# Kernel optimization log

Hardware: AMD Instinct MI355X
Metric: run time of the kernel (lower is better)

The kernel has to match this reference:

```python
import jax, jax.numpy as jnp
import numpy as np

B, S, D, H, G = 2, 4096, 768, 12, 64
HD = D // H
W = 256              # one-sided window (attention_window=512); also the chunk size
NC = S // W
NEG = -1e9
SCALE = 1.0 / np.sqrt(HD)


def setup_inputs() -> dict:
    key = jax.random.key(0)
    ks = jax.random.split(key, 9)
    lin = lambda k: 0.02 * jax.random.normal(k, (D, D), dtype=jnp.float32)
    zb = lambda: jnp.zeros((D,), jnp.float32)
    return {
        "query": jax.random.normal(ks[0], (S, B, D), dtype=jnp.float32),
        # 0 = local token, -1 = global token (wrapper multiplies by -1 -> +1 = global in HF convention)
        "key_padding_mask": jnp.zeros((B, S), jnp.int32).at[:, :G].set(-1),
        "Wq": lin(ks[1]), "bq": zb(),
        "Wk": lin(ks[2]), "bk": zb(),
        "Wv": lin(ks[3]), "bv": zb(),
        "Wqg": lin(ks[4]), "bqg": zb(),
        "Wkg": lin(ks[5]), "bkg": zb(),
        "Wvg": lin(ks[6]), "bvg": zb(),
        "Wo": lin(ks[7]), "bo": zb(),
    }


def _heads(x):  # [B,S,D] -> [B,H,S,HD]
    return x.reshape(B, S, H, HD).transpose(0, 2, 1, 3)


def reference(query, key_padding_mask, Wq, bq, Wk, bk, Wv, bv,
              Wqg, bqg, Wkg, bkg, Wvg, bvg, Wo, bo):
    x = query.transpose(1, 0, 2)                      # [B,S,D]
    attn_mask = -key_padding_mask                     # wrapper: key_padding_mask * -1
    is_pad = attn_mask < 0                            # [B,S]
    is_glb = attn_mask > 0

    q = _heads(x @ Wq + bq) * SCALE                   # [B,H,S,HD]
    k = _heads(x @ Wk + bk)
    v = _heads(x @ Wv + bv)

    # ---- sliding-window scores via overlapping 3-chunk key blocks ----
    qc = q.reshape(B, H, NC, W, HD)
    blk_idx = jnp.arange(NC)[:, None] * W + jnp.arange(3 * W)[None, :]   # [NC,3W] into padded seq
    kpad = jnp.pad(k, ((0, 0), (0, 0), (W, W), (0, 0)))
    vpad = jnp.pad(v, ((0, 0), (0, 0), (W, W), (0, 0)))
    kblk = kpad[:, :, blk_idx]                        # [B,H,NC,3W,HD]
    vblk = vpad[:, :, blk_idx]
    local = jnp.einsum('bhcqd,bhckd->bhcqk', qc, kblk)  # [B,H,NC,W,3W]

    rel = jnp.arange(3 * W)[None, :] - jnp.arange(W)[:, None] - W        # key pos - query pos
    jpos = (jnp.arange(NC)[:, None, None] - 1) * W + jnp.arange(3 * W)[None, None, :]
    band_ok = (jnp.abs(rel)[None] <= W) & (jpos >= 0) & (jpos < S)       # [NC,W,3W]

    key_bad = is_pad | is_glb                         # pad keys masked; global keys handled separately
    kb_blk = jnp.pad(key_bad, ((0, 0), (W, W)), constant_values=True)[:, blk_idx]  # [B,NC,3W]
    ok = band_ok[None, None] & ~kb_blk[:, None, :, None, :]
    local = jnp.where(ok, local, NEG)

    # ---- all queries -> global keys (first G tokens), regular K/V ----
    gsc = jnp.einsum('bhqd,bhgd->bhqg', q, k[:, :, :G])                  # [B,H,S,G]

    scores = jnp.concatenate([gsc, local.reshape(B, H, S, 3 * W)], axis=-1)
    probs = jax.nn.softmax(scores, axis=-1)
    pg = probs[..., :G]
    pl = probs[..., G:].reshape(B, H, NC, W, 3 * W)

    out = jnp.einsum('bhcqk,bhckd->bhcqd', pl, vblk).reshape(B, H, S, HD)
    out = out + jnp.einsum('bhqg,bhgd->bhqd', pg, v[:, :, :G])

    # ---- global query rows: full attention with the dedicated global projections ----
    qg = (_heads(x @ Wqg + bqg) * SCALE)[:, :, :G]    # [B,H,G,HD]
    kg = _heads(x @ Wkg + bkg)
    vg = _heads(x @ Wvg + bvg)
    gq = jnp.einsum('bhgd,bhkd->bhgk', qg, kg)        # [B,H,G,S]
    gq = jnp.where(is_pad[:, None, None, :], NEG, gq)
    gp = jax.nn.softmax(gq, axis=-1)
    out = out.at[:, :, :G].set(jnp.einsum('bhgk,bhkd->bhgd', gp, vg))

    attn_out = out.transpose(0, 2, 1, 3).reshape(B, S, D)   # merge heads -> [B,S,D]
    attn_out = attn_out.transpose(1, 0, 2)                  # back to [S,B,D]
    return attn_out @ Wo + bo                               # wrapper's output Linear
```

## Files before the change

kernel.cpp:

```cpp
#include <hip/hip_runtime.h>
#include <hip/hip_bf16.h>
#include <cstdint>

#define BB 2
#define SS 4096
#define DD 768
#define HH 12
#define GG 64
#define WW 256

typedef __hip_bfloat16 bf16;
typedef unsigned short u16;
typedef __attribute__((ext_vector_type(8))) short short8v;
typedef __attribute__((ext_vector_type(4))) float floatx4;
typedef __attribute__((ext_vector_type(16))) float floatx16;

#define QSCALE 0.18033688011112042f

__device__ __forceinline__ float b2f(u16 u) {
  return __uint_as_float(((unsigned int)u) << 16);
}
__device__ __forceinline__ u16 f2bu(float f) {
  bf16 h = __float2bfloat16(f);
  return *reinterpret_cast<u16*>(&h);
}
__device__ __forceinline__ void async_copy16(const u16* g, u16* l) {
  __builtin_amdgcn_global_load_lds(
      (const __attribute__((address_space(1))) void*)g,
      (__attribute__((address_space(3))) void*)l, 16, 0, 0);
}

struct P7 { const void* p[7]; };

__global__ __launch_bounds__(256) void detect_dtype(const u16* __restrict__ q,
                                                    int* __restrict__ flag) {
  __shared__ int cnt;
  int tid = threadIdx.x;
  if (tid == 0) cnt = 0;
  __syncthreads();
  int bad = 0;
#pragma unroll
  for (int i = 0; i < 16; ++i) {
    float f = b2f(q[tid * 16 + i]);
    if (!isfinite(f) || fabsf(f) > 100.f) bad++;
  }
  atomicAdd(&cnt, bad);
  __syncthreads();
  if (tid == 0) *flag = (cnt > 256) ? 1 : 0;
}

__global__ __launch_bounds__(256) void prep(P7 wsrc, P7 bsrc,
                                            const void* __restrict__ qsrc,
                                            bf16* __restrict__ cWt,
                                            bf16* __restrict__ cB,
                                            bf16* __restrict__ cQ,
                                            const int* __restrict__ flag) {
  bool f32 = (*flag != 0);
  int z = blockIdx.z;
  if (z < 7) {
    __shared__ float tile[32][33];
    const void* src = wsrc.p[z];
    bf16* d = cWt + (size_t)z * DD * DD;
    int tx = threadIdx.x & 31, ty = threadIdx.x >> 5;
    int k0 = blockIdx.x * 32, n0 = blockIdx.y * 32;
#pragma unroll
    for (int i = 0; i < 32; i += 8) {
      int k = k0 + ty + i, n = n0 + tx;
      float v = f32 ? ((const float*)src)[(size_t)k * DD + n]
                    : b2f(((const u16*)src)[(size_t)k * DD + n]);
      tile[ty + i][tx] = v;
    }
    __syncthreads();
#pragma unroll
    for (int i = 0; i < 32; i += 8) {
      int n = n0 + ty + i, k = k0 + tx;
      d[(size_t)n * DD + k] = __float2bfloat16(tile[tx][ty + i]);
    }
  } else if (z == 7) {
    int bidx = blockIdx.x + 24 * blockIdx.y;
    const int n = BB * HH * SS * 64;
    for (int i = bidx * 256 + threadIdx.x; i < n; i += 576 * 256) {
      float v = f32 ? ((const float*)qsrc)[i] : b2f(((const u16*)qsrc)[i]);
      cQ[i] = __float2bfloat16(v);
    }
  } else {
    int which = blockIdx.x;
    if (which >= 7 || blockIdx.y != 0) return;
    const void* s = bsrc.p[which];
    for (int j = threadIdx.x; j < DD; j += 256)
      cB[which * DD + j] =
          __float2bfloat16(f32 ? ((const float*)s)[j] : b2f(((const u16*)s)[j]));
  }
}

__global__ __launch_bounds__(256) void tr_vt2(const bf16* __restrict__ s0,
                                              bf16* __restrict__ d0,
                                              const bf16* __restrict__ s1,
                                              bf16* __restrict__ d1) {
  __shared__ u16 T[64][66];
  int stile = blockIdx.x, bh = blockIdx.y;
  const u16* in = (const u16*)(blockIdx.z ? s1 : s0) + (size_t)bh * SS * 64;
  u16* out = (u16*)(blockIdx.z ? d1 : d0) + (size_t)bh * SS * 64;
  int tid = threadIdx.x;
  int srow = tid >> 2, scol = (tid & 3) * 16;
#pragma unroll
  for (int i = 0; i < 4; ++i) {
    ushort4 u = *(const ushort4*)(in + (size_t)(stile * 64 + srow) * 64 + scol + 4 * i);
    *(ushort2*)&T[srow][scol + 4 * i] = make_ushort2(u.x, u.y);
    *(ushort2*)&T[srow][scol + 4 * i + 2] = make_ushort2(u.z, u.w);
  }
  __syncthreads();
#pragma unroll
  for (int i = 0; i < 4; ++i) {
    ushort4 u;
    u.x = T[scol + 4 * i + 0][srow];
    u.y = T[scol + 4 * i + 1][srow];
    u.z = T[scol + 4 * i + 2][srow];
    u.w = T[scol + 4 * i + 3][srow];
    *(ushort4*)(out + (size_t)srow * SS + stile * 64 + scol + 4 * i) = u;
  }
}

__device__ __forceinline__ short8v lda(u16 (*Ls)[64], int base, int lane, int kk) {
  int row = base + (lane & 31);
  int c = (kk >> 3) + (lane >> 5);
  return *(const short8v*)&Ls[row][((c ^ (row & 7)) << 3)];
}

__device__ __forceinline__ void gemm_core3(const u16* __restrict__ Xp,
                                           const u16* __restrict__ Wp, int bm,
                                           int bn, int tid, u16 (*As)[64],
                                           u16 (*Bs)[64], floatx16 (&acc)[4][2]) {
  int lane = tid & 63, w = tid >> 6;
  int wm = w * 64;
  int r8 = lane >> 3;
  int sw = (((lane & 7) ^ (r8 & 7)) << 3);
  for (int k0 = 0; k0 < DD; k0 += 64) {
    __syncthreads();
#pragma unroll
    for (int j = 0; j < 4; ++j)
      async_copy16(Wp + (size_t)(bn + w * 32 + j * 8 + r8) * DD + k0 + sw,
                   &As[w * 32 + j * 8][0]);
#pragma unroll
    for (int j = 0; j < 8; ++j)
      async_copy16(Xp + (size_t)(bm + w * 64 + j * 8 + r8) * DD + k0 + sw,
                   &Bs[w * 64 + j * 8][0]);
    __syncthreads();
#pragma unroll
    for (int kk = 0; kk < 64; kk += 16) {
      short8v a[4], b[2];
#pragma unroll
      for (int nf = 0; nf < 4; ++nf) a[nf] = lda(As, nf * 32, lane, kk);
#pragma unroll
      for (int mf = 0; mf < 2; ++mf) b[mf] = lda(Bs, wm + mf * 32, lane, kk);
#pragma unroll
      for (int nf = 0; nf < 4; ++nf)
#pragma unroll
        for (int mf = 0; mf < 2; ++mf)
          acc[nf][mf] = __builtin_amdgcn_mfma_f32_32x32x16_bf16(
              a[nf], b[mf], acc[nf][mf], 0, 0, 0);
    }
  }
}

__device__ __forceinline__ void gemm_core2(const u16* __restrict__ Xp,
                                           const u16* __restrict__ Wp, int bm,
                                           int bn, int tid, u16 (*As)[64],
                                           u16 (*Bs)[64], floatx16 (&acc)[2][2]) {
  int lane = tid & 63, w = tid >> 6;
  int wm = (w >> 1) * 64, wn = (w & 1) * 64;
  int r8 = lane >> 3;
  int sw = (((lane & 7) ^ (r8 & 7)) << 3);
  for (int k0 = 0; k0 < DD; k0 += 64) {
    __syncthreads();
#pragma unroll
    for (int j = 0; j < 4; ++j) {
      async_copy16(Wp + (size_t)(bn + w * 32 + j * 8 + r8) * DD + k0 + sw,
                   &As[w * 32 + j * 8][0]);
      async_copy16(Xp + (size_t)(bm + w * 32 + j * 8 + r8) * DD + k0 + sw,
                   &Bs[w * 32 + j * 8][0]);
    }
    __syncthreads();
#pragma unroll
    for (int kk = 0; kk < 64; kk += 16) {
      short8v a0 = lda(As, wn, lane, kk);
      short8v a1 = lda(As, wn + 32, lane, kk);
      short8v b0 = lda(Bs, wm, lane, kk);
      short8v b1 = lda(Bs, wm + 32, lane, kk);
      acc[0][0] = __builtin_amdgcn_mfma_f32_32x32x16_bf16(a0, b0, acc[0][0], 0, 0, 0);
      acc[0][1] = __builtin_amdgcn_mfma_f32_32x32x16_bf16(a0, b1, acc[0][1], 0, 0, 0);
      acc[1][0] = __builtin_amdgcn_mfma_f32_32x32x16_bf16(a1, b0, acc[1][0], 0, 0, 0);
      acc[1][1] = __builtin_amdgcn_mfma_f32_32x32x16_bf16(a1, b1, acc[1][1], 0, 0, 0);
    }
  }
}

__global__ __launch_bounds__(256, 2) void gemm5(const bf16* __restrict__ Xb,
                                                const bf16* __restrict__ Wt0,
                                                const bf16* __restrict__ b0,
                                                bf16* __restrict__ out0,
                                                bf16* __restrict__ qg) {
  __shared__ __align__(16) u16 As[128][64];
  __shared__ __align__(16) u16 Bs[256][64];
  int tid = threadIdx.x, lane = tid & 63, w = tid >> 6;
  int which, bn, bm;
  if (blockIdx.y == 30) {
    if (blockIdx.x >= 6) return;
    which = 5;
    bn = blockIdx.x * 128;
    bm = 0;
  } else {
    which = blockIdx.y / 6;
    bn = (blockIdx.y % 6) * 128;
    bm = blockIdx.x * 256;
  }
  const u16* Wp = (const u16*)Wt0 + (size_t)which * DD * DD;
  const u16* bias = (const u16*)b0 + which * DD;
  int Sdim = (which == 5) ? GG : SS;
  u16* outp = (which == 5) ? (u16*)qg
                           : (u16*)out0 + (size_t)which * BB * HH * SS * 64;
  float scale = (which == 0 || which == 5) ? QSCALE : 1.f;
  floatx16 acc[4][2];
#pragma unroll
  for (int i = 0; i < 4; ++i)
#pragma unroll
    for (int j = 0; j < 2; ++j) acc[i][j] = (floatx16)(0.f);
  gemm_core3((const u16*)Xb, Wp, bm, bn, tid, As, Bs, acc);
#pragma unroll
  for (int nf = 0; nf < 4; ++nf) {
#pragma unroll
    for (int g = 0; g < 4; ++g) {
      int nbase = bn + nf * 32 + g * 8 + ((lane >> 5) << 2);
      int h = nbase >> 6, nsub = nbase & 63;
      ushort4 bi = *(const ushort4*)&bias[nbase];
#pragma unroll
      for (int mf = 0; mf < 2; ++mf) {
        int m = bm + w * 64 + mf * 32 + (lane & 31);
        int s = m >> 1, b = m & 1;
        if (which == 5 && s >= GG) continue;
        ushort4 o;
        o.x = f2bu((acc[nf][mf][4 * g + 0] + b2f(bi.x)) * scale);
        o.y = f2bu((acc[nf][mf][4 * g + 1] + b2f(bi.y)) * scale);
        o.z = f2bu((acc[nf][mf][4 * g + 2] + b2f(bi.z)) * scale);
        o.w = f2bu((acc[nf][mf][4 * g + 3] + b2f(bi.w)) * scale);
        *(ushort4*)(outp + ((size_t)(b * HH + h) * Sdim + s) * 64 + nsub) = o;
      }
    }
  }
}

__global__ __launch_bounds__(256, 4) void gemm_out(const bf16* __restrict__ Xb,
                                                   const bf16* __restrict__ Wtb,
                                                   const bf16* __restrict__ biasb,
                                                   float* __restrict__ outv) {
  __shared__ __align__(16) u16 As[128][64];
  __shared__ __align__(16) u16 Bs[128][64];
  int tid = threadIdx.x, lane = tid & 63, w = tid >> 6;
  int wm = (w >> 1) * 64, wn = (w & 1) * 64;
  int bm = blockIdx.x * 128, bn = blockIdx.y * 128;
  floatx16 acc[2][2];
#pragma unroll
  for (int i = 0; i < 2; ++i)
#pragma unroll
    for (int j = 0; j < 2; ++j) acc[i][j] = (floatx16)(0.f);
  gemm_core2((const u16*)Xb, (const u16*)Wtb, bm, bn, tid, As, Bs, acc);
  const u16* bias = (const u16*)biasb;
#pragma unroll
  for (int nt = 0; nt < 2; ++nt) {
    int n0 = bn + wn + nt * 32 + ((lane >> 5) << 2);
    ushort4 bi[4];
#pragma unroll
    for (int g = 0; g < 4; ++g) bi[g] = *(const ushort4*)&bias[n0 + g * 8];
#pragma unroll
    for (int mt = 0; mt < 2; ++mt) {
      int m = bm + wm + mt * 32 + (lane & 31);
      float* outb = outv + (size_t)m * DD + n0;
#pragma unroll
      for (int g = 0; g < 4; ++g) {
        float4 o;
        o.x = acc[nt][mt][4 * g + 0] + b2f(bi[g].x);
        o.y = acc[nt][mt][4 * g + 1] + b2f(bi[g].y);
        o.z = acc[nt][mt][4 * g + 2] + b2f(bi[g].z);
        o.w = acc[nt][mt][4 * g + 3] + b2f(bi[g].w);
        *(float4*)(outb + g * 8) = o;
      }
    }
  }
}

__global__ __launch_bounds__(256, 3) void attn_local128(
    const bf16* __restrict__ qb, const bf16* __restrict__ kb,
    const bf16* __restrict__ vtb, const int* __restrict__ kpm,
    bf16* __restrict__ attnout) {
  __shared__ __align__(16) u16 Qs[128][64];
  __shared__ __align__(16) u16 Ks[64][64];
  __shared__ __align__(16) u16 Vt[64][64];
  __shared__ __align__(16) u16 Ps[128][72];
  __shared__ float Ls[128];
  __shared__ int kbadS[64];
  int bid = blockIdx.x;
  int tile = bid & 31, bh = bid >> 5;
  int b = bh / HH, h = bh % HH;
  int tid = threadIdx.x, lane = tid & 63, w = tid >> 6;
  int quad = lane >> 4, t = lane & 15;
  const u16* qp = (const u16*)qb + (size_t)bh * SS * 64;
  const u16* kp = (const u16*)kb + (size_t)bh * SS * 64;
  const u16* vp = (const u16*)vtb + (size_t)bh * SS * 64;
  int sq0 = GG + tile * 128;
#pragma unroll
  for (int j = 0; j < 4; ++j) {
    int qr = sq0 + w * 32 + j * 8 + (lane >> 3);
    int sr = qr < SS ? qr : SS - 1;
    async_copy16(qp + (size_t)sr * 64 + (lane & 7) * 8, &Qs[w * 32 + j * 8][0]);
  }
  __syncthreads();
  short8v aq[2][2];
#pragma unroll
  for (int st = 0; st < 2; ++st)
#pragma unroll
    for (int ks = 0; ks < 2; ++ks)
      aq[st][ks] = *(const short8v*)&Qs[w * 32 + st * 16 + t][ks * 32 + quad * 8];
  floatx4 O[2][4];
#pragma unroll
  for (int st = 0; st < 2; ++st)
#pragma unroll
    for (int dt = 0; dt < 4; ++dt) O[st][dt] = (floatx4)(0.f);
  float ps[2][4] = {};
  int win_lo = max(sq0 - WW, GG);
  int win_hi = min(sq0 + 127 + WW, SS - 1);
  int kb_lo = win_lo & ~63;
  int iters = ((win_hi - kb_lo) >> 6) + 2;
  for (int it = 0; it < iters; ++it) {
    int kbs = (it == 0) ? 0 : kb_lo + ((it - 1) << 6);
    __syncthreads();
#pragma unroll
    for (int j = 0; j < 2; ++j) {
      async_copy16(kp + (size_t)(kbs + w * 16 + j * 8 + (lane >> 3)) * 64 +
                       (lane & 7) * 8,
                   &Ks[w * 16 + j * 8][0]);
      async_copy16(vp + (size_t)(w * 16 + j * 8 + (lane >> 3)) * SS + kbs +
                       (lane & 7) * 8,
                   &Vt[w * 16 + j * 8][0]);
    }
    if (tid < 64) kbadS[tid] = kpm[b * SS + kbs + tid];
    __syncthreads();
#pragma unroll
    for (int st = 0; st < 2; ++st) {
      floatx4 S[4];
#pragma unroll
      for (int nt = 0; nt < 4; ++nt) {
        S[nt] = (floatx4)(0.f);
#pragma unroll
        for (int ks = 0; ks < 2; ++ks) {
          short8v bk = *(const short8v*)&Ks[nt * 16 + t][ks * 32 + quad * 8];
          S[nt] = __builtin_amdgcn_mfma_f32_16x16x32_bf16(aq[st][ks], bk, S[nt],
                                                          0, 0, 0);
        }
      }
      int prow = w * 32 + st * 16 + quad * 4;
      if (it == 0) {
#pragma unroll
        for (int nt = 0; nt < 4; ++nt)
#pragma unroll
          for (int r = 0; r < 4; ++r) {
            float p = exp2f(S[nt][r]);
            ps[st][r] += p;
            Ps[prow + r][((nt ^ quad) << 4) + t] = f2bu(p);
          }
      } else {
#pragma unroll
        for (int r = 0; r < 4; ++r) {
          int qr = sq0 + prow + r;
          int off = kbs + t + WW - qr;
#pragma unroll
          for (int nt = 0; nt < 4; ++nt) {
            int bad = kbadS[nt * 16 + t];
            unsigned u = (unsigned)(off + nt * 16);
            float p = exp2f((u <= 2 * WW && bad == 0) ? S[nt][r] : -3.0e38f);
            ps[st][r] += p;
            Ps[prow + r][((nt ^ quad) << 4) + t] = f2bu(p);
          }
        }
      }
    }
    short8v ap[2][2];
#pragma unroll
    for (int st = 0; st < 2; ++st)
#pragma unroll
      for (int ks = 0; ks < 2; ++ks) {
        int chunk = (2 * ks + (quad >> 1)) ^ ((t >> 2) & 3);
        ap[st][ks] = *(const short8v*)&Ps[w * 32 + st * 16 + t]
                                        [(chunk << 4) + ((quad & 1) << 3)];
      }
#pragma unroll
    for (int dt = 0; dt < 4; ++dt) {
#pragma unroll
      for (int ks = 0; ks < 2; ++ks) {
        short8v av = *(const short8v*)&Vt[dt * 16 + t][ks * 32 + quad * 8];
#pragma unroll
        for (int st = 0; st < 2; ++st)
          O[st][dt] = __builtin_amdgcn_mfma_f32_16x16x32_bf16(av, ap[st][ks],
                                                              O[st][dt], 0, 0, 0);
      }
    }
  }
#pragma unroll
  for (int st = 0; st < 2; ++st) {
#pragma unroll
    for (int r = 0; r < 4; ++r)
#pragma unroll
      for (int off = 1; off < 16; off <<= 1) ps[st][r] += __shfl_xor(ps[st][r], off);
    if (t == 0)
#pragma unroll
      for (int r = 0; r < 4; ++r) Ls[w * 32 + st * 16 + quad * 4 + r] = ps[st][r];
  }
#pragma unroll
  for (int st = 0; st < 2; ++st) {
    int q = sq0 + w * 32 + st * 16 + t;
    if (q < SS) {
      float linv = 1.0f / Ls[w * 32 + st * 16 + t];
#pragma unroll
      for (int dt = 0; dt < 4; ++dt) {
        ushort4 o;
        o.x = f2bu(O[st][dt][0] * linv);
        o.y = f2bu(O[st][dt][1] * linv);
        o.z = f2bu(O[st][dt][2] * linv);
        o.w = f2bu(O[st][dt][3] * linv);
        *(ushort4*)((u16*)attnout + ((size_t)q * BB + b) * DD + h * 64 +
                    dt * 16 + quad * 4) = o;
      }
    }
  }
}

__global__ __launch_bounds__(256) void attn_glb(
    const bf16* __restrict__ qgb, const bf16* __restrict__ kgb,
    const bf16* __restrict__ vtb, const int* __restrict__ kpm,
    float* __restrict__ part) {
  __shared__ __align__(16) u16 Qs[64][72];
  __shared__ __align__(16) u16 Ks[64][72];
  __shared__ __align__(16) u16 Vt[64][72];
  __shared__ __align__(16) u16 Ps[64][72];
  __shared__ int kbadS[64];
  int bid = blockIdx.x;
  int bh = bid >> 4, seg = bid & 15;
  int b = bh / HH;
  int tid = threadIdx.x, lane = tid & 63, w = tid >> 6;
  int quad = lane >> 4, t = lane & 15;
  const u16* qp = (const u16*)qgb + (size_t)bh * GG * 64;
  const u16* kp = (const u16*)kgb + (size_t)bh * SS * 64;
  const u16* vp = (const u16*)vtb + (size_t)bh * SS * 64;
  int srow = tid >> 2, scol = (tid & 3) * 16;
#pragma unroll
  for (int i = 0; i < 4; ++i)
    *(ushort4*)&Qs[srow][scol + 4 * i] =
        *(const ushort4*)(qp + (size_t)srow * 64 + scol + 4 * i);
  __syncthreads();
  short8v aq[2];
#pragma unroll
  for (int ks = 0; ks < 2; ++ks)
    aq[ks] = *(const short8v*)&Qs[16 * w + t][ks * 32 + quad * 8];
  floatx4 O[4];
#pragma unroll
  for (int i = 0; i < 4; ++i) O[i] = (floatx4)(0.f);
  float ps[4] = {0.f, 0.f, 0.f, 0.f};
  for (int it = 0; it < 4; ++it) {
    int kbs = (seg << 8) + (it << 6);
    ushort4 ku[4], vu[4];
#pragma unroll
    for (int i = 0; i < 4; ++i) {
      ku[i] = *(const ushort4*)(kp + (size_t)(kbs + srow) * 64 + scol + 4 * i);
      vu[i] = *(const ushort4*)(vp + (size_t)srow * SS + kbs + scol + 4 * i);
    }
    int kbval = (tid < 64) ? kpm[b * SS + kbs + tid] : 0;
    __syncthreads();
#pragma unroll
    for (int i = 0; i < 4; ++i) {
      *(ushort4*)&Ks[srow][scol + 4 * i] = ku[i];
      *(ushort4*)&Vt[srow][scol + 4 * i] = vu[i];
    }
    if (tid < 64) kbadS[tid] = kbval;
    __syncthreads();
    floatx4 S[4];
#pragma unroll
    for (int nt = 0; nt < 4; ++nt) {
      S[nt] = (floatx4)(0.f);
#pragma unroll
      for (int ks = 0; ks < 2; ++ks) {
        short8v bk = *(const short8v*)&Ks[nt * 16 + t][ks * 32 + quad * 8];
        S[nt] = __builtin_amdgcn_mfma_f32_16x16x32_bf16(aq[ks], bk, S[nt], 0, 0, 0);
      }
    }
#pragma unroll
    for (int nt = 0; nt < 4; ++nt) {
      int bad = kbadS[nt * 16 + t];
#pragma unroll
      for (int r = 0; r < 4; ++r) {
        float p = exp2f((bad <= 0) ? S[nt][r] : -3.0e38f);
        ps[r] += p;
        Ps[16 * w + quad * 4 + r][((nt ^ quad) << 4) + t] = f2bu(p);
      }
    }
    short8v ap[2];
#pragma unroll
    for (int ks = 0; ks < 2; ++ks) {
      int chunk = (2 * ks + (quad >> 1)) ^ ((t >> 2) & 3);
      ap[ks] = *(const short8v*)&Ps[16 * w + t][(chunk << 4) + ((quad & 1) << 3)];
    }
#pragma unroll
    for (int dt = 0; dt < 4; ++dt)
#pragma unroll
      for (int ks = 0; ks < 2; ++ks) {
        short8v bv = *(const short8v*)&Vt[dt * 16 + t][ks * 32 + quad * 8];
        O[dt] = __builtin_amdgcn_mfma_f32_16x16x32_bf16(ap[ks], bv, O[dt], 0, 0, 0);
      }
  }
#pragma unroll
  for (int r = 0; r < 4; ++r)
#pragma unroll
    for (int off = 1; off < 16; off <<= 1) ps[r] += __shfl_xor(ps[r], off);
  float* pO = part + (size_t)bid * 4160;
#pragma unroll
  for (int dt = 0; dt < 4; ++dt)
#pragma unroll
    for (int r = 0; r < 4; ++r)
      pO[(16 * w + quad * 4 + r) * 64 + dt * 16 + t] = O[dt][r];
  if (t == 0)
#pragma unroll
    for (int r = 0; r < 4; ++r) pO[4096 + 16 * w + quad * 4 + r] = ps[r];
}

__global__ __launch_bounds__(256) void attn_comb(const float* __restrict__ part,
                                                 bf16* __restrict__ attnout) {
  int tid = threadIdx.x, lane = tid & 63, w = tid >> 6;
  int idx = blockIdx.x * 4 + w;
  int bh = idx >> 6, row = idx & 63;
  int b = bh / HH, h = bh % HH;
  float o = 0.f, L = 0.f;
#pragma unroll
  for (int s16 = 0; s16 < 16; ++s16) {
    const float* p = part + (size_t)(bh * 16 + s16) * 4160;
    o += p[(row << 6) + lane];
    L += p[4096 + row];
  }
  attnout[((size_t)row * BB + b) * DD + h * 64 + lane] = __float2bfloat16(o / L);
}

extern "C" void kernel_launch(void* const* d_in, const int* in_sizes, int n_in,
                              void* d_out, int out_size, void* d_ws,
                              size_t ws_size, hipStream_t stream) {
  const int* kpm = (const int*)d_in[1];
  float* outp = (float*)d_out;
  const size_t SZ = (size_t)BB * HH * SS * 64;
  const size_t WSZ = (size_t)DD * DD;
  bf16* p = (bf16*)d_ws;
  bf16* cQ = p; p += SZ;
  bf16* cWt = p; p += 7 * WSZ;
  bf16* cB = p; p += 7 * DD;
  bf16* q = p; p += SZ;
  bf16* k = p; p += SZ;
  bf16* v = p; p += SZ;
  bf16* kg = p; p += SZ;
  bf16* vg = p; p += SZ;
  bf16* qg = p; p += (size_t)BB * HH * GG * 64;
  bf16* attnout = p; p += SZ;
  float* part = (float*)p;
  int* flag = (int*)(part + (size_t)384 * 4160);
  bf16* vT = cQ;
  bf16* vgT = v;
  dim3 blk(256);
  (void)kg; (void)vg;

  P7 wsrc{{d_in[2], d_in[4], d_in[6], d_in[10], d_in[12], d_in[8], d_in[14]}};
  P7 bsrc{{d_in[3], d_in[5], d_in[7], d_in[11], d_in[13], d_in[9], d_in[15]}};

  detect_dtype<<<1, blk, 0, stream>>>((const u16*)d_in[0], flag);
  prep<<<dim3(24, 24, 9), blk, 0, stream>>>(wsrc, bsrc, d_in[0], cWt, cB, cQ, flag);
  gemm5<<<dim3(32, 31), blk, 0, stream>>>(cQ, cWt, cB, q, qg);
  tr_vt2<<<dim3(64, 24, 2), blk, 0, stream>>>(v, vT, vg, vgT);
  attn_local128<<<dim3(24 * 32), blk, 0, stream>>>(q, k, vT, kpm, attnout);
  attn_glb<<<dim3(BB * HH * 16), blk, 0, stream>>>(qg, kg, vgT, kpm, part);
  attn_comb<<<dim3(BB * HH * 16), blk, 0, stream>>>(part, attnout);
  gemm_out<<<dim3(64, 6), blk, 0, stream>>>(attnout, cWt + 6 * WSZ, cB + 6 * DD, outp);
}
```

Baseline: 295.7 us.

## Retile projection GEMM to 128x128 with LDS-staged coalesced head-layout stores

The fused QKV/global projection kernel moves from 256x128 tiles at two blocks per CU to 128x128 tiles at four blocks per CU. It also uses a flattened 1D grid, which removes the idle blocks that previously exited early. The epilogue now adds bias, scales and converts the accumulators into a shared-memory tile, then writes full 64-element head rows so global stores are contiguous. The aim is higher occupancy, better load balance and less scattered store traffic. The cost is less operand reuse per tile and extra LDS round trips and barriers in the epilogue.

```diff
diff --git a/kernel.cpp b/kernel.cpp
--- a/kernel.cpp
+++ b/kernel.cpp
@@ -127,42 +127,6 @@
   return *(const short8v*)&Ls[row][((c ^ (row & 7)) << 3)];
 }
 
-__device__ __forceinline__ void gemm_core3(const u16* __restrict__ Xp,
-                                           const u16* __restrict__ Wp, int bm,
-                                           int bn, int tid, u16 (*As)[64],
-                                           u16 (*Bs)[64], floatx16 (&acc)[4][2]) {
-  int lane = tid & 63, w = tid >> 6;
-  int wm = w * 64;
-  int r8 = lane >> 3;
-  int sw = (((lane & 7) ^ (r8 & 7)) << 3);
-  for (int k0 = 0; k0 < DD; k0 += 64) {
-    __syncthreads();
-#pragma unroll
-    for (int j = 0; j < 4; ++j)
-      async_copy16(Wp + (size_t)(bn + w * 32 + j * 8 + r8) * DD + k0 + sw,
-                   &As[w * 32 + j * 8][0]);
-#pragma unroll
-    for (int j = 0; j < 8; ++j)
-      async_copy16(Xp + (size_t)(bm + w * 64 + j * 8 + r8) * DD + k0 + sw,
-                   &Bs[w * 64 + j * 8][0]);
-    __syncthreads();
-#pragma unroll
-    for (int kk = 0; kk < 64; kk += 16) {
-      short8v a[4], b[2];
-#pragma unroll
-      for (int nf = 0; nf < 4; ++nf) a[nf] = lda(As, nf * 32, lane, kk);
-#pragma unroll
-      for (int mf = 0; mf < 2; ++mf) b[mf] = lda(Bs, wm + mf * 32, lane, kk);
-#pragma unroll
-      for (int nf = 0; nf < 4; ++nf)
-#pragma unroll
-        for (int mf = 0; mf < 2; ++mf)
-          acc[nf][mf] = __builtin_amdgcn_mfma_f32_32x32x16_bf16(
-              a[nf], b[mf], acc[nf][mf], 0, 0, 0);
-    }
-  }
-}
-
 __device__ __forceinline__ void gemm_core2(const u16* __restrict__ Xp,
                                            const u16* __restrict__ Wp, int bm,
                                            int bn, int tid, u16 (*As)[64],
@@ -195,56 +159,70 @@
   }
 }
 
-__global__ __launch_bounds__(256, 2) void gemm5(const bf16* __restrict__ Xb,
-                                                const bf16* __restrict__ Wt0,
-                                                const bf16* __restrict__ b0,
-                                                bf16* __restrict__ out0,
-                                                bf16* __restrict__ qg) {
-  __shared__ __align__(16) u16 As[128][64];
-  __shared__ __align__(16) u16 Bs[256][64];
+__global__ __launch_bounds__(256, 4) void gemm5c(const bf16* __restrict__ Xb,
+                                                 const bf16* __restrict__ Wt0,
+                                                 const bf16* __restrict__ bset,
+                                                 bf16* __restrict__ out0,
+                                                 bf16* __restrict__ qgp) {
+  __shared__ __align__(16) u16 SH[16384];
+  u16 (*As)[64] = (u16(*)[64])SH;
+  u16 (*Bs)[64] = (u16(*)[64])(SH + 8192);
   int tid = threadIdx.x, lane = tid & 63, w = tid >> 6;
-  int which, bn, bm;
-  if (blockIdx.y == 30) {
-    if (blockIdx.x >= 6) return;
-    which = 5;
-    bn = blockIdx.x * 128;
-    bm = 0;
+  int wg = blockIdx.x;
+  int which, bm, bn;
+  if (wg >= 1920) {
+    which = 5; bm = 0; bn = (wg - 1920) * 128;
   } else {
-    which = blockIdx.y / 6;
-    bn = (blockIdx.y % 6) * 128;
-    bm = blockIdx.x * 256;
+    which = wg / 384;
+    int rem = wg % 384;
+    bm = (rem / 6) * 128;
+    bn = (rem % 6) * 128;
   }
   const u16* Wp = (const u16*)Wt0 + (size_t)which * DD * DD;
-  const u16* bias = (const u16*)b0 + which * DD;
+  const u16* bias = (const u16*)bset + which * DD;
   int Sdim = (which == 5) ? GG : SS;
-  u16* outp = (which == 5) ? (u16*)qg
+  u16* outp = (which == 5) ? (u16*)qgp
                            : (u16*)out0 + (size_t)which * BB * HH * SS * 64;
   float scale = (which == 0 || which == 5) ? QSCALE : 1.f;
-  floatx16 acc[4][2];
-#pragma unroll
-  for (int i = 0; i < 4; ++i)
+
+  floatx16 acc[2][2];
+#pragma unroll
+  for (int i = 0; i < 2; ++i)
 #pragma unroll
     for (int j = 0; j < 2; ++j) acc[i][j] = (floatx16)(0.f);
-  gemm_core3((const u16*)Xb, Wp, bm, bn, tid, As, Bs, acc);
-#pragma unroll
-  for (int nf = 0; nf < 4; ++nf) {
-#pragma unroll
-    for (int g = 0; g < 4; ++g) {
-      int nbase = bn + nf * 32 + g * 8 + ((lane >> 5) << 2);
-      int h = nbase >> 6, nsub = nbase & 63;
-      ushort4 bi = *(const ushort4*)&bias[nbase];
-#pragma unroll
-      for (int mf = 0; mf < 2; ++mf) {
-        int m = bm + w * 64 + mf * 32 + (lane & 31);
-        int s = m >> 1, b = m & 1;
-        if (which == 5 && s >= GG) continue;
+  gemm_core2((const u16*)Xb, Wp, bm, bn, tid, As, Bs, acc);
+
+  const int CST = 132;
+  u16* Cs = SH;
+  int wn = (w & 1) << 6, wmh = (w >> 1) << 5;
+#pragma unroll
+  for (int mt = 0; mt < 2; ++mt) {
+    __syncthreads();
+#pragma unroll
+    for (int nt = 0; nt < 2; ++nt)
+#pragma unroll
+      for (int g = 0; g < 4; ++g) {
+        int ncol = wn + nt * 32 + g * 8 + ((lane >> 5) << 2);
+        ushort4 bi = *(const ushort4*)&bias[bn + ncol];
+        int crow = wmh + (lane & 31);
         ushort4 o;
-        o.x = f2bu((acc[nf][mf][4 * g + 0] + b2f(bi.x)) * scale);
-        o.y = f2bu((acc[nf][mf][4 * g + 1] + b2f(bi.y)) * scale);
-        o.z = f2bu((acc[nf][mf][4 * g + 2] + b2f(bi.z)) * scale);
-        o.w = f2bu((acc[nf][mf][4 * g + 3] + b2f(bi.w)) * scale);
-        *(ushort4*)(outp + ((size_t)(b * HH + h) * Sdim + s) * 64 + nsub) = o;
-      }
+        o.x = f2bu((acc[nt][mt][4 * g + 0] + b2f(bi.x)) * scale);
+        o.y = f2bu((acc[nt][mt][4 * g + 1] + b2f(bi.y)) * scale);
+        o.z = f2bu((acc[nt][mt][4 * g + 2] + b2f(bi.z)) * scale);
+        o.w = f2bu((acc[nt][mt][4 * g + 3] + b2f(bi.w)) * scale);
+        *(ushort4*)&Cs[crow * CST + ncol] = o;
+      }
+    __syncthreads();
+#pragma unroll
+    for (int j = 0; j < 8; ++j) {
+      int c = j * 256 + tid;
+      int ch = c & 15, mh = c >> 4;
+      int mloc = mh >> 1, hloc = mh & 1;
+      int m = bm + ((mloc >> 5) << 6) + mt * 32 + (mloc & 31);
+      int s = m >> 1, b = m & 1;
+      int h = (bn >> 6) + hloc;
+      ushort4 vv = *(const ushort4*)&Cs[mloc * CST + hloc * 64 + ch * 4];
+      *(ushort4*)(outp + ((size_t)(b * HH + h) * Sdim + s) * 64 + ch * 4) = vv;
     }
   }
 }
@@ -576,7 +554,7 @@
 
   detect_dtype<<<1, blk, 0, stream>>>((const u16*)d_in[0], flag);
   prep<<<dim3(24, 24, 9), blk, 0, stream>>>(wsrc, bsrc, d_in[0], cWt, cB, cQ, flag);
-  gemm5<<<dim3(32, 31), blk, 0, stream>>>(cQ, cWt, cB, q, qg);
+  gemm5c<<<dim3(5 * 384 + 6), blk, 0, stream>>>(cQ, cWt, cB, q, qg);
   tr_vt2<<<dim3(64, 24, 2), blk, 0, stream>>>(v, vT, vg, vgT);
   attn_local128<<<dim3(24 * 32), blk, 0, stream>>>(q, k, vT, kpm, attnout);
   attn_glb<<<dim3(BB * HH * 16), blk, 0, stream>>>(qg, kg, vgT, kpm, part);
```

After: 285.4 us. -3.5%, faster.
